# Performance work log

Hardware: AMD Instinct MI355X
Metric: run time of the kernel (lower is better)

The kernel has to match this reference:

```python
import jax, jax.numpy as jnp
import numpy as np

DIM, HEADS, WH, WW, MLAT, MLON = 512, 8, 8, 8, 32, 64
N = WH * WW
B = MLAT * MLON
PER_LAT = (2 * WH - 1) * (2 * WW - 1)  # 225


def _make_rel_idx():
    # Swin 2D relative position index inside one window
    ch, cw = np.arange(WH), np.arange(WW)
    coords = np.stack(np.meshgrid(ch, cw, indexing='ij')).reshape(2, -1)  # (2, N)
    rel = coords[:, :, None] - coords[:, None, :]                          # (2, N, N)
    rel = rel.transpose(1, 2, 0).astype(np.int64)
    rel[..., 0] += WH - 1
    rel[..., 1] += WW - 1
    rel[..., 0] *= 2 * WW - 1
    idx2d = rel.sum(-1)                                                    # (N, N)
    # earth-specific: each lat row i gets its own 225-entry slab; lon diff is 0
    idx = idx2d[None] + np.arange(MLAT)[:, None, None] * PER_LAT           # (Mlat, N, N)
    idx = np.broadcast_to(idx[:, None], (MLAT, MLON, N, N)).reshape(B, N, N)
    return jnp.asarray(idx.astype(np.int32))


def setup_inputs() -> dict:
    key = jax.random.key(0)
    k = jax.random.split(key, 5)
    x = jax.random.normal(k[0], (B, N, DIM), dtype=jnp.float32)
    w_qkv = jax.random.normal(k[1], (3 * DIM, DIM), dtype=jnp.float32) * 0.02
    b_qkv = jnp.zeros((3 * DIM,), dtype=jnp.float32)
    w_proj = jax.random.normal(k[2], (DIM, DIM), dtype=jnp.float32) * 0.02
    b_proj = jnp.zeros((DIM,), dtype=jnp.float32)
    bias_table = jax.random.normal(k[3], (MLAT * PER_LAT, HEADS), dtype=jnp.float32) * 0.02
    return {
        'x': x, 'w_qkv': w_qkv, 'b_qkv': b_qkv,
        'w_proj': w_proj, 'b_proj': b_proj,
        'bias_table': bias_table, 'rel_idx': _make_rel_idx(),
    }


def reference(x, w_qkv, b_qkv, w_proj, b_proj, bias_table, rel_idx):
    Bn, Nn, C = x.shape
    D = C // HEADS
    qkv = (x @ w_qkv.T + b_qkv).reshape(Bn, Nn, 3, HEADS, D)
    q = jnp.transpose(qkv[:, :, 0], (0, 2, 1, 3))  # (B, H, N, D)
    k = jnp.transpose(qkv[:, :, 1], (0, 2, 1, 3))
    v = jnp.transpose(qkv[:, :, 2], (0, 2, 1, 3))
    # gather learned earth bias: (B, N, N, H) -> (B, H, N, N)
    bias = jnp.transpose(bias_table[rel_idx], (0, 3, 1, 2))
    scale = D ** -0.5  # SDPA default scale (qk_scale is None)
    attn = jax.nn.softmax(jnp.einsum('bhnd,bhmd->bhnm', q, k) * scale + bias, axis=-1)
    out = jnp.einsum('bhnm,bhmd->bhnd', attn, v)
    out = jnp.transpose(out, (0, 2, 1, 3)).reshape(Bn, Nn, C)
    return out @ w_proj.T + b_proj
```

## Files before the change

kernel.cpp:

```cpp
#include <hip/hip_runtime.h>
#include <stdint.h>

typedef __attribute__((ext_vector_type(8))) short short8;
typedef __attribute__((ext_vector_type(4))) short short4v;
typedef __attribute__((ext_vector_type(4))) float float4v;

__device__ __forceinline__ short f2bf(float f) {
  uint32_t u = __builtin_bit_cast(uint32_t, f);
  u += 0x7FFFu + ((u >> 16) & 1u);
  return (short)(u >> 16);
}

#define XPITCH 520
#define QPITCH 72

__global__ void prep_weights(const float* __restrict__ wq, const float* __restrict__ wp,
                             short* __restrict__ wq_b, short* __restrict__ wp_b) {
  int i = blockIdx.x * blockDim.x + threadIdx.x;
  int stride = gridDim.x * blockDim.x;
  for (int j = i; j < 786432 / 4; j += stride) {
    float4 v = ((const float4*)wq)[j];
    short4v t = {f2bf(v.x), f2bf(v.y), f2bf(v.z), f2bf(v.w)};
    ((short4v*)wq_b)[j] = t;
  }
  for (int j = i; j < 262144 / 4; j += stride) {
    float4 v = ((const float4*)wp)[j];
    short4v t = {f2bf(v.x), f2bf(v.y), f2bf(v.z), f2bf(v.w)};
    ((short4v*)wp_b)[j] = t;
  }
}

__global__ __launch_bounds__(512, 2)
void qkv_attn(const float* __restrict__ x, const short* __restrict__ wq,
              const float* __restrict__ bqkv, const float* __restrict__ btab,
              short* __restrict__ attn) {
  __shared__ short Xs[64 * XPITCH];
  __shared__ short Qs[2][64 * QPITCH];
  __shared__ short Ks[2][64 * QPITCH];
  __shared__ short Vt[2][64 * QPITCH];

  const int b    = blockIdx.x;
  const int tid  = threadIdx.x;
  const int lane = tid & 63;
  const int w    = tid >> 6;
  const int l16  = lane & 15;
  const int quad = lane >> 4;
  const int lat  = b >> 6;

  const float* xw = x + (size_t)b * (64 * 512);
  for (int c = tid; c < 64 * 128; c += 512) {
    int n = c >> 7, kc = c & 127;
    float4 v = *(const float4*)(xw + n * 512 + kc * 4);
    short4v t = {f2bf(v.x), f2bf(v.y), f2bf(v.z), f2bf(v.w)};
    *(short4v*)&Xs[n * XPITCH + kc * 4] = t;
  }
  __syncthreads();

  for (int h0 = 0; h0 < 8; h0 += 2) {
    for (int s = w; s < 24; s += 8) {
      const int hsel  = s / 12;
      const int rem   = s % 12;
      const int mat   = rem >> 2;
      const int strip = rem & 3;
      const int h     = h0 + hsel;
      const short* Wbase = wq + (mat * 512 + h * 64 + strip * 16) * 512;

      float4v acc[4] = {};
      if (mat < 2) {
        const short* Arow = Wbase + l16 * 512 + quad * 8;
        for (int kk = 0; kk < 512; kk += 32) {
          short8 a = *(const short8*)(Arow + kk);
#pragma unroll
          for (int t = 0; t < 4; ++t) {
            short8 bf = *(const short8*)&Xs[(t * 16 + l16) * XPITCH + kk + quad * 8];
            acc[t] = __builtin_amdgcn_mfma_f32_16x16x32_bf16(a, bf, acc[t], 0, 0, 0);
          }
        }
        float bias[4];
#pragma unroll
        for (int i = 0; i < 4; ++i)
          bias[i] = bqkv[mat * 512 + h * 64 + strip * 16 + quad * 4 + i];
        short* dst = (mat == 0) ? &Qs[hsel][0] : &Ks[hsel][0];
        const float scale = (mat == 0) ? 0.125f : 1.0f;
#pragma unroll
        for (int t = 0; t < 4; ++t) {
          int n = t * 16 + l16;
          short4v pk;
#pragma unroll
          for (int i = 0; i < 4; ++i) pk[i] = f2bf((acc[t][i] + bias[i]) * scale);
          *(short4v*)&dst[n * QPITCH + strip * 16 + quad * 4] = pk;
        }
      } else {
        const short* Brow = Wbase + l16 * 512 + quad * 8;
        for (int kk = 0; kk < 512; kk += 32) {
          short8 bf = *(const short8*)(Brow + kk);
#pragma unroll
          for (int t = 0; t < 4; ++t) {
            short8 a = *(const short8*)&Xs[(t * 16 + l16) * XPITCH + kk + quad * 8];
            acc[t] = __builtin_amdgcn_mfma_f32_16x16x32_bf16(a, bf, acc[t], 0, 0, 0);
          }
        }
        float bias = bqkv[1024 + h * 64 + strip * 16 + l16];
#pragma unroll
        for (int t = 0; t < 4; ++t) {
          short4v pk;
#pragma unroll
          for (int i = 0; i < 4; ++i) pk[i] = f2bf(acc[t][i] + bias);
          *(short4v*)&Vt[hsel][(strip * 16 + l16) * QPITCH + t * 16 + quad * 4] = pk;
        }
      }
    }
    __syncthreads();

    {
      const int hsel = w >> 2;
      const int h    = h0 + hsel;
      const int n0   = (w & 3) * 16;

      float4v s4[4] = {};
#pragma unroll
      for (int kd = 0; kd < 64; kd += 32) {
        short8 a = *(const short8*)&Qs[hsel][(n0 + l16) * QPITCH + kd + quad * 8];
#pragma unroll
        for (int t = 0; t < 4; ++t) {
          short8 bf = *(const short8*)&Ks[hsel][(t * 16 + l16) * QPITCH + kd + quad * 8];
          s4[t] = __builtin_amdgcn_mfma_f32_16x16x32_bf16(a, bf, s4[t], 0, 0, 0);
        }
      }
#pragma unroll
      for (int t = 0; t < 4; ++t) {
        int m = t * 16 + l16;
#pragma unroll
        for (int i = 0; i < 4; ++i) {
          int n = n0 + quad * 4 + i;
          int idx = ((n >> 3) - (m >> 3) + 7) * 15 + ((n & 7) - (m & 7) + 7) + lat * 225;
          s4[t][i] += btab[idx * 8 + h];
        }
      }
      float p[4][4];
#pragma unroll
      for (int i = 0; i < 4; ++i) {
        float mx = fmaxf(fmaxf(s4[0][i], s4[1][i]), fmaxf(s4[2][i], s4[3][i]));
        mx = fmaxf(mx, __shfl_xor(mx, 1));
        mx = fmaxf(mx, __shfl_xor(mx, 2));
        mx = fmaxf(mx, __shfl_xor(mx, 4));
        mx = fmaxf(mx, __shfl_xor(mx, 8));
        float e0 = __expf(s4[0][i] - mx), e1 = __expf(s4[1][i] - mx);
        float e2 = __expf(s4[2][i] - mx), e3 = __expf(s4[3][i] - mx);
        float sm = e0 + e1 + e2 + e3;
        sm += __shfl_xor(sm, 1);
        sm += __shfl_xor(sm, 2);
        sm += __shfl_xor(sm, 4);
        sm += __shfl_xor(sm, 8);
        float inv = 1.0f / sm;
        p[0][i] = e0 * inv; p[1][i] = e1 * inv; p[2][i] = e2 * inv; p[3][i] = e3 * inv;
      }
#pragma unroll
      for (int t = 0; t < 4; ++t)
#pragma unroll
        for (int i = 0; i < 4; ++i)
          Qs[hsel][(n0 + quad * 4 + i) * QPITCH + t * 16 + l16] = f2bf(p[t][i]);
      __syncthreads();

      float4v o4[4] = {};
#pragma unroll
      for (int km = 0; km < 64; km += 32) {
        short8 a = *(const short8*)&Qs[hsel][(n0 + l16) * QPITCH + km + quad * 8];
#pragma unroll
        for (int t = 0; t < 4; ++t) {
          short8 bf = *(const short8*)&Vt[hsel][(t * 16 + l16) * QPITCH + km + quad * 8];
          o4[t] = __builtin_amdgcn_mfma_f32_16x16x32_bf16(a, bf, o4[t], 0, 0, 0);
        }
      }
      short* ob = attn + (size_t)b * (64 * 512);
#pragma unroll
      for (int t = 0; t < 4; ++t)
#pragma unroll
        for (int i = 0; i < 4; ++i)
          ob[(n0 + quad * 4 + i) * 512 + h * 64 + t * 16 + l16] = f2bf(o4[t][i]);
    }
    __syncthreads();
  }
}

__global__ __launch_bounds__(256, 3)
void proj_gemm(const short* __restrict__ attn, const short* __restrict__ wp,
               const float* __restrict__ bproj, float* __restrict__ out) {
  __shared__ short As[128 * 32];
  __shared__ short Bs[128 * 32];
  const int n0   = blockIdx.x * 128;
  const int m0   = blockIdx.y * 128;
  const int tid  = threadIdx.x;
  const int lane = tid & 63;
  const int w    = tid >> 6;
  const int l16  = lane & 15;
  const int quad = lane >> 4;
  const int wm   = w >> 1, wn = w & 1;

  float4v acc[4][4] = {};

  for (int kk = 0; kk < 512; kk += 32) {
#pragma unroll
    for (int r = 0; r < 2; ++r) {
      int c = tid + r * 256;
      int row = c >> 2, kc = c & 3;
      *(uint4*)&As[c * 8] = *(const uint4*)(attn + (size_t)(m0 + row) * 512 + kk + kc * 8);
      *(uint4*)&Bs[c * 8] = *(const uint4*)(wp + (size_t)(n0 + row) * 512 + kk + kc * 8);
    }
    __syncthreads();
    short8 a[4], bf[4];
#pragma unroll
    for (int ti = 0; ti < 4; ++ti)
      a[ti] = *(const short8*)&As[(wm * 64 + ti * 16 + l16) * 32 + quad * 8];
#pragma unroll
    for (int tj = 0; tj < 4; ++tj)
      bf[tj] = *(const short8*)&Bs[(wn * 64 + tj * 16 + l16) * 32 + quad * 8];
#pragma unroll
    for (int ti = 0; ti < 4; ++ti)
#pragma unroll
      for (int tj = 0; tj < 4; ++tj)
        acc[ti][tj] = __builtin_amdgcn_mfma_f32_16x16x32_bf16(a[ti], bf[tj], acc[ti][tj], 0, 0, 0);
    __syncthreads();
  }

  float bj[4];
#pragma unroll
  for (int tj = 0; tj < 4; ++tj) bj[tj] = bproj[n0 + wn * 64 + tj * 16 + l16];
#pragma unroll
  for (int ti = 0; ti < 4; ++ti)
#pragma unroll
    for (int i = 0; i < 4; ++i) {
      size_t rowoff = (size_t)(m0 + wm * 64 + ti * 16 + quad * 4 + i) * 512;
#pragma unroll
      for (int tj = 0; tj < 4; ++tj)
        out[rowoff + n0 + wn * 64 + tj * 16 + l16] = acc[ti][tj][i] + bj[tj];
    }
}

extern "C" void kernel_launch(void* const* d_in, const int* in_sizes, int n_in,
                              void* d_out, int out_size, void* d_ws, size_t ws_size,
                              hipStream_t stream) {
  const float* x     = (const float*)d_in[0];
  const float* wqkv  = (const float*)d_in[1];
  const float* bqkv  = (const float*)d_in[2];
  const float* wproj = (const float*)d_in[3];
  const float* bproj = (const float*)d_in[4];
  const float* btab  = (const float*)d_in[5];
  float* out = (float*)d_out;

  short* wq_b = (short*)d_ws;
  short* wp_b = wq_b + 786432;
  short* attn = wp_b + 262144;

  prep_weights<<<256, 256, 0, stream>>>(wqkv, wproj, wq_b, wp_b);
  qkv_attn<<<2048, 512, 0, stream>>>(x, wq_b, bqkv, btab, attn);
  proj_gemm<<<dim3(4, 1024), 256, 0, stream>>>(attn, wp_b, bproj, out);
}
```

Measured before the change: 1.035 ms.

## Share X fragments across fused Q/K/V MFMAs and use direct global-to-LDS loads in projection

In the QKV stage each wave now computes one Q, one K and one V strip together, so every X fragment read from LDS feeds twelve MFMAs instead of four, which cuts LDS traffic and removes the per-strip branching. A __syncthreads between the softmax write to LDS and the P·V MFMA is removed. That looks safe only because each wave writes and reads its own 16 rows, though the P tile goes through shared memory. The projection GEMM switches to a K-tile of 64, uses global_load_lds async copies into LDS, remaps the 1D grid for L2 locality, and lowers the occupancy hint from 3 to 2 blocks.

```diff
diff --git a/kernel.cpp b/kernel.cpp
--- a/kernel.cpp
+++ b/kernel.cpp
@@ -9,6 +9,12 @@
   uint32_t u = __builtin_bit_cast(uint32_t, f);
   u += 0x7FFFu + ((u >> 16) & 1u);
   return (short)(u >> 16);
+}
+
+__device__ __forceinline__ void gl_lds16(const short* g, short* l) {
+  __builtin_amdgcn_global_load_lds(
+      (const __attribute__((address_space(1))) unsigned int*)g,
+      (__attribute__((address_space(3))) unsigned int*)l, 16, 0, 0);
 }
 
 #define XPITCH 520
@@ -56,58 +62,72 @@
   }
   __syncthreads();
 
+  const int g  = w >> 2;
+  const int st = w & 3;
+
   for (int h0 = 0; h0 < 8; h0 += 2) {
-    for (int s = w; s < 24; s += 8) {
-      const int hsel  = s / 12;
-      const int rem   = s % 12;
-      const int mat   = rem >> 2;
-      const int strip = rem & 3;
-      const int h     = h0 + hsel;
-      const short* Wbase = wq + (mat * 512 + h * 64 + strip * 16) * 512;
-
-      float4v acc[4] = {};
-      if (mat < 2) {
-        const short* Arow = Wbase + l16 * 512 + quad * 8;
-        for (int kk = 0; kk < 512; kk += 32) {
-          short8 a = *(const short8*)(Arow + kk);
-#pragma unroll
-          for (int t = 0; t < 4; ++t) {
-            short8 bf = *(const short8*)&Xs[(t * 16 + l16) * XPITCH + kk + quad * 8];
-            acc[t] = __builtin_amdgcn_mfma_f32_16x16x32_bf16(a, bf, acc[t], 0, 0, 0);
-          }
-        }
-        float bias[4];
-#pragma unroll
-        for (int i = 0; i < 4; ++i)
-          bias[i] = bqkv[mat * 512 + h * 64 + strip * 16 + quad * 4 + i];
-        short* dst = (mat == 0) ? &Qs[hsel][0] : &Ks[hsel][0];
-        const float scale = (mat == 0) ? 0.125f : 1.0f;
-#pragma unroll
-        for (int t = 0; t < 4; ++t) {
-          int n = t * 16 + l16;
-          short4v pk;
-#pragma unroll
-          for (int i = 0; i < 4; ++i) pk[i] = f2bf((acc[t][i] + bias[i]) * scale);
-          *(short4v*)&dst[n * QPITCH + strip * 16 + quad * 4] = pk;
-        }
-      } else {
-        const short* Brow = Wbase + l16 * 512 + quad * 8;
-        for (int kk = 0; kk < 512; kk += 32) {
-          short8 bf = *(const short8*)(Brow + kk);
-#pragma unroll
-          for (int t = 0; t < 4; ++t) {
-            short8 a = *(const short8*)&Xs[(t * 16 + l16) * XPITCH + kk + quad * 8];
-            acc[t] = __builtin_amdgcn_mfma_f32_16x16x32_bf16(a, bf, acc[t], 0, 0, 0);
-          }
-        }
-        float bias = bqkv[1024 + h * 64 + strip * 16 + l16];
-#pragma unroll
-        for (int t = 0; t < 4; ++t) {
-          short4v pk;
-#pragma unroll
-          for (int i = 0; i < 4; ++i) pk[i] = f2bf(acc[t][i] + bias);
-          *(short4v*)&Vt[hsel][(strip * 16 + l16) * QPITCH + t * 16 + quad * 4] = pk;
-        }
+    {
+      const int hq = h0 + g;
+      const int hk = h0 + 1 - g;
+      const short* Aq = wq + (size_t)((hq * 64 + st * 16 + l16) * 512) + quad * 8;
+      const short* Ak = wq + (size_t)(((512) + hk * 64 + st * 16 + l16) * 512) + quad * 8;
+      const short* Av = wq + (size_t)(((1024) + hq * 64 + st * 16 + l16) * 512) + quad * 8;
+      const short* xb0 = &Xs[l16 * XPITCH + quad * 8];
+      const short* xb1 = xb0 + 16 * XPITCH;
+      const short* xb2 = xb0 + 32 * XPITCH;
+      const short* xb3 = xb0 + 48 * XPITCH;
+
+      float4v aQ[4] = {}, aK[4] = {}, aV[4] = {};
+#pragma unroll 4
+      for (int kk = 0; kk < 512; kk += 32) {
+        short8 wqf = *(const short8*)(Aq + kk);
+        short8 wkf = *(const short8*)(Ak + kk);
+        short8 wvf = *(const short8*)(Av + kk);
+        short8 x0 = *(const short8*)(xb0 + kk);
+        short8 x1 = *(const short8*)(xb1 + kk);
+        short8 x2 = *(const short8*)(xb2 + kk);
+        short8 x3 = *(const short8*)(xb3 + kk);
+        aQ[0] = __builtin_amdgcn_mfma_f32_16x16x32_bf16(wqf, x0, aQ[0], 0, 0, 0);
+        aQ[1] = __builtin_amdgcn_mfma_f32_16x16x32_bf16(wqf, x1, aQ[1], 0, 0, 0);
+        aQ[2] = __builtin_amdgcn_mfma_f32_16x16x32_bf16(wqf, x2, aQ[2], 0, 0, 0);
+        aQ[3] = __builtin_amdgcn_mfma_f32_16x16x32_bf16(wqf, x3, aQ[3], 0, 0, 0);
+        aK[0] = __builtin_amdgcn_mfma_f32_16x16x32_bf16(wkf, x0, aK[0], 0, 0, 0);
+        aK[1] = __builtin_amdgcn_mfma_f32_16x16x32_bf16(wkf, x1, aK[1], 0, 0, 0);
+        aK[2] = __builtin_amdgcn_mfma_f32_16x16x32_bf16(wkf, x2, aK[2], 0, 0, 0);
+        aK[3] = __builtin_amdgcn_mfma_f32_16x16x32_bf16(wkf, x3, aK[3], 0, 0, 0);
+        aV[0] = __builtin_amdgcn_mfma_f32_16x16x32_bf16(x0, wvf, aV[0], 0, 0, 0);
+        aV[1] = __builtin_amdgcn_mfma_f32_16x16x32_bf16(x1, wvf, aV[1], 0, 0, 0);
+        aV[2] = __builtin_amdgcn_mfma_f32_16x16x32_bf16(x2, wvf, aV[2], 0, 0, 0);
+        aV[3] = __builtin_amdgcn_mfma_f32_16x16x32_bf16(x3, wvf, aV[3], 0, 0, 0);
+      }
+
+      float bq[4], bk[4];
+#pragma unroll
+      for (int i = 0; i < 4; ++i) {
+        bq[i] = bqkv[hq * 64 + st * 16 + quad * 4 + i];
+        bk[i] = bqkv[512 + hk * 64 + st * 16 + quad * 4 + i];
+      }
+      short* dq = &Qs[g][0];
+      short* dk = &Ks[1 - g][0];
+#pragma unroll
+      for (int t = 0; t < 4; ++t) {
+        int n = t * 16 + l16;
+        short4v pq, pk;
+#pragma unroll
+        for (int i = 0; i < 4; ++i) {
+          pq[i] = f2bf((aQ[t][i] + bq[i]) * 0.125f);
+          pk[i] = f2bf(aK[t][i] + bk[i]);
+        }
+        *(short4v*)&dq[n * QPITCH + st * 16 + quad * 4] = pq;
+        *(short4v*)&dk[n * QPITCH + st * 16 + quad * 4] = pk;
+      }
+      float bv = bqkv[1024 + hq * 64 + st * 16 + l16];
+#pragma unroll
+      for (int t = 0; t < 4; ++t) {
+        short4v pv;
+#pragma unroll
+        for (int i = 0; i < 4; ++i) pv[i] = f2bf(aV[t][i] + bv);
+        *(short4v*)&Vt[g][(st * 16 + l16) * QPITCH + t * 16 + quad * 4] = pv;
       }
     }
     __syncthreads();
@@ -160,7 +180,6 @@
 #pragma unroll
         for (int i = 0; i < 4; ++i)
           Qs[hsel][(n0 + quad * 4 + i) * QPITCH + t * 16 + l16] = f2bf(p[t][i]);
-      __syncthreads();
 
       float4v o4[4] = {};
 #pragma unroll
@@ -183,13 +202,17 @@
   }
 }
 
-__global__ __launch_bounds__(256, 3)
+__global__ __launch_bounds__(256, 2)
 void proj_gemm(const short* __restrict__ attn, const short* __restrict__ wp,
                const float* __restrict__ bproj, float* __restrict__ out) {
-  __shared__ short As[128 * 32];
-  __shared__ short Bs[128 * 32];
-  const int n0   = blockIdx.x * 128;
-  const int m0   = blockIdx.y * 128;
+  __shared__ short As[128 * 64];
+  __shared__ short Bs[128 * 64];
+
+  const int orig = blockIdx.x;
+  const int wg   = (orig & 7) * 512 + (orig >> 3);
+  const int n0   = (wg & 3) * 128;
+  const int m0   = (wg >> 2) * 128;
+
   const int tid  = threadIdx.x;
   const int lane = tid & 63;
   const int w    = tid >> 6;
@@ -197,29 +220,35 @@
   const int quad = lane >> 4;
   const int wm   = w >> 1, wn = w & 1;
 
+  const int srow = lane >> 3;
+  const int scol = (lane & 7) * 8;
+
   float4v acc[4][4] = {};
 
-  for (int kk = 0; kk < 512; kk += 32) {
-#pragma unroll
-    for (int r = 0; r < 2; ++r) {
-      int c = tid + r * 256;
-      int row = c >> 2, kc = c & 3;
-      *(uint4*)&As[c * 8] = *(const uint4*)(attn + (size_t)(m0 + row) * 512 + kk + kc * 8);
-      *(uint4*)&Bs[c * 8] = *(const uint4*)(wp + (size_t)(n0 + row) * 512 + kk + kc * 8);
-    }
-    __syncthreads();
-    short8 a[4], bf[4];
-#pragma unroll
-    for (int ti = 0; ti < 4; ++ti)
-      a[ti] = *(const short8*)&As[(wm * 64 + ti * 16 + l16) * 32 + quad * 8];
-#pragma unroll
-    for (int tj = 0; tj < 4; ++tj)
-      bf[tj] = *(const short8*)&Bs[(wn * 64 + tj * 16 + l16) * 32 + quad * 8];
-#pragma unroll
-    for (int ti = 0; ti < 4; ++ti)
+  for (int kk = 0; kk < 512; kk += 64) {
+#pragma unroll
+    for (int j = 0; j < 4; ++j) {
+      int chunk = w * 4 + j;
+      int row = chunk * 8 + srow;
+      gl_lds16(attn + (size_t)(m0 + row) * 512 + kk + scol, &As[chunk * 512]);
+      gl_lds16(wp + (size_t)(n0 + row) * 512 + kk + scol, &Bs[chunk * 512]);
+    }
+    __syncthreads();
+#pragma unroll
+    for (int ks = 0; ks < 64; ks += 32) {
+      short8 a[4], bf[4];
+#pragma unroll
+      for (int ti = 0; ti < 4; ++ti)
+        a[ti] = *(const short8*)&As[(wm * 64 + ti * 16 + l16) * 64 + ks + quad * 8];
 #pragma unroll
       for (int tj = 0; tj < 4; ++tj)
-        acc[ti][tj] = __builtin_amdgcn_mfma_f32_16x16x32_bf16(a[ti], bf[tj], acc[ti][tj], 0, 0, 0);
+        bf[tj] = *(const short8*)&Bs[(wn * 64 + tj * 16 + l16) * 64 + ks + quad * 8];
+#pragma unroll
+      for (int ti = 0; ti < 4; ++ti)
+#pragma unroll
+        for (int tj = 0; tj < 4; ++tj)
+          acc[ti][tj] = __builtin_amdgcn_mfma_f32_16x16x32_bf16(a[ti], bf[tj], acc[ti][tj], 0, 0, 0);
+    }
     __syncthreads();
   }
 
@@ -254,5 +283,5 @@
 
   prep_weights<<<256, 256, 0, stream>>>(wqkv, wproj, wq_b, wp_b);
   qkv_attn<<<2048, 512, 0, stream>>>(x, wq_b, bqkv, btab, attn);
-  proj_gemm<<<dim3(4, 1024), 256, 0, stream>>>(attn, wp_b, bproj, out);
-}
+  proj_gemm<<<4096, 256, 0, stream>>>(attn, wp_b, bproj, out);
+}
```

After: 1.063 ms. +2.7%, slower.
